# Kernel optimization log

Measured on AMD Instinct MI355X. Metric: run time of the kernel, lower is better.

## Reference

```python
import jax, jax.numpy as jnp
import numpy as np


def _rope_tables(N, d, base=10000.0):
    # LLaMA-style: freqs over even dims, interleaved (pairs) layout
    inv = 1.0 / (base ** (np.arange(0, d, 2)[: d // 2].astype(np.float32) / d))
    ang = np.outer(np.arange(N, dtype=np.float32), inv)  # [N, d/2]
    return jnp.asarray(np.cos(ang), jnp.float32), jnp.asarray(np.sin(ang), jnp.float32)


def _apply_rope(x, cos, sin):
    # x: [B, h, N, d]; pairs layout (..., d/2, 2)
    B, h, N, d = x.shape
    xs = x.reshape(B, h, N, d // 2, 2)
    x0, x1 = xs[..., 0], xs[..., 1]
    c = cos[None, None, :, :]
    s = sin[None, None, :, :]
    o0 = x0 * c - x1 * s
    o1 = x1 * c + x0 * s
    return jnp.stack([o0, o1], axis=-1).reshape(B, h, N, d)


def _neighborhood_attn(q, k, v, window, scale):
    # q,k,v: [B, h, H, W, d]; NATTEN-style clamped window of size window x window
    B, h, H, W, d = q.shape
    r = window // 2
    ih = jnp.clip(jnp.arange(H) - r, 0, H - window)[:, None] + jnp.arange(window)  # [H, w]
    iw = jnp.clip(jnp.arange(W) - r, 0, W - window)[:, None] + jnp.arange(window)  # [W, w]
    # gather windows: [B, h, H, W, w, w, d]
    kwin = k[:, :, ih[:, None, :, None], iw[None, :, None, :], :]
    vwin = v[:, :, ih[:, None, :, None], iw[None, :, None, :], :]
    attn = jnp.einsum('bhijd,bhijpqd->bhijpq', q, kwin) * scale
    attn = jax.nn.softmax(attn.reshape(B, h, H, W, window * window), axis=-1)
    out = jnp.einsum('bhijp,bhijpd->bhijd', attn,
                     vwin.reshape(B, h, H, W, window * window, d))
    return out  # [B, h, H, W, d]


def setup_inputs() -> dict:
    key = jax.random.key(0)
    k1, k2, k3 = jax.random.split(key, 3)
    B, H, W, C = 2, 56, 56, 256
    N = H * W
    x = jax.random.normal(k1, (B, N, C), dtype=jnp.float32)
    Wqkv = jax.random.normal(k2, (C, 3 * C), dtype=jnp.float32) * 0.02
    Wproj = jax.random.normal(k3, (C, C), dtype=jnp.float32) * 0.02
    bproj = jnp.zeros((C,), dtype=jnp.float32)
    return {"x": x, "Wqkv": Wqkv, "Wproj": Wproj, "bproj": bproj, "H": H, "W": W}


def reference(x, Wqkv, Wproj, bproj, H, W):
    head_dim = 32
    window = 7
    B, N, C = x.shape
    heads = C // head_dim
    scale = head_dim ** (-0.5)

    qkv = (x @ Wqkv).reshape(B, N, 3, heads, head_dim)
    qkv = jnp.transpose(qkv, (2, 0, 3, 1, 4))  # [3, B, h, N, d]
    q, k, v = qkv[0], qkv[1], qkv[2]

    cos, sin = _rope_tables(N, head_dim)
    q = _apply_rope(q, cos, sin)
    k = _apply_rope(k, cos, sin)

    q = q.reshape(B, heads, H, W, head_dim)
    k = k.reshape(B, heads, H, W, head_dim)
    v = v.reshape(B, heads, H, W, head_dim)

    out = _neighborhood_attn(q, k, v, window, scale)  # [B, h, H, W, d]
    out = out.reshape(B, heads, N, head_dim)
    out = jnp.transpose(out, (0, 2, 1, 3)).reshape(B, N, C)
    return out @ Wproj + bproj
```

## Files before the change

### kernel.cpp

```cpp
#include <hip/hip_runtime.h>
#include <hip/hip_bf16.h>

#define HH 56
#define WW 56
#define NPOS 3136
#define BATCH 2
#define HEADS 8

typedef __attribute__((ext_vector_type(4))) float floatx4;
typedef __attribute__((ext_vector_type(8))) short short8;

static __device__ __forceinline__ ushort f2b(float f) {
    __hip_bfloat16 h = __float2bfloat16(f);
    return *reinterpret_cast<ushort*>(&h);
}
static __device__ __forceinline__ float b2f(ushort u) {
    return __uint_as_float(((uint)u) << 16);
}

static __device__ __forceinline__ void async16(const ushort* g, ushort* l) {
    __builtin_amdgcn_global_load_lds(
        (const __attribute__((address_space(1))) unsigned int*)g,
        (__attribute__((address_space(3))) unsigned int*)l, 16, 0, 0);
}

__constant__ float INVF[16] = {
    1.0f,   0.5623413251903491f,   0.31622776601683794f,   0.17782794100389228f,
    0.1f,   0.05623413251903491f,  0.031622776601683794f,  0.017782794100389228f,
    0.01f,  0.005623413251903491f, 0.0031622776601683794f, 0.0017782794100389228f,
    0.001f, 0.0005623413251903491f,0.00031622776601683794f,0.00017782794100389228f
};


__global__ __launch_bounds__(256) void prepass(
    const float* __restrict__ x, const float* __restrict__ wqkv,
    const float* __restrict__ wproj,
    ushort* __restrict__ xb, ushort* __restrict__ wqkvT,
    ushort* __restrict__ wprojT, float* __restrict__ ropeT)
{
    __shared__ ushort Ls[64 * 65];
    const int bid = blockIdx.x, t = threadIdx.x;
    if (bid < 1568) {
        int i = (bid * 256 + t) * 4;
        float4 v = *(const float4*)&x[i];
        ushort4 h; h.x = f2b(v.x); h.y = f2b(v.y); h.z = f2b(v.z); h.w = f2b(v.w);
        *(ushort4*)&xb[i] = h;
    } else if (bid < 1764) {
        int i = (bid - 1568) * 256 + t;
        int pos = i >> 4, pr = i & 15;
        float s, c;
        __sincosf((float)pos * INVF[pr], &s, &c);
        ropeT[2 * i] = c; ropeT[2 * i + 1] = s;
    } else if (bid < 1812) {
        int l = bid - 1764;
        int nb = (l % 12) * 64, kb = (l / 12) * 64;
#pragma unroll
        for (int i = 0; i < 16; ++i) {
            int e = t + 256 * i, kk = e >> 6, nn = e & 63;
            Ls[kk * 65 + nn] = f2b(wqkv[(size_t)(kb + kk) * 768 + nb + nn]);
        }
        __syncthreads();
#pragma unroll
        for (int i = 0; i < 16; ++i) {
            int e = t + 256 * i, nn = e >> 6, kk = e & 63;
            wqkvT[(size_t)(nb + nn) * 256 + kb + kk] = Ls[kk * 65 + nn];
        }
    } else {
        int l = bid - 1812;
        int nb = (l & 3) * 64, kb = (l >> 2) * 64;
#pragma unroll
        for (int i = 0; i < 16; ++i) {
            int e = t + 256 * i, kk = e >> 6, nn = e & 63;
            Ls[kk * 65 + nn] = f2b(wproj[(size_t)(kb + kk) * 256 + nb + nn]);
        }
        __syncthreads();
#pragma unroll
        for (int i = 0; i < 16; ++i) {
            int e = t + 256 * i, nn = e >> 6, kk = e & 63;
            wprojT[(size_t)(nb + nn) * 256 + kb + kk] = Ls[kk * 65 + nn];
        }
    }
}

__global__ __launch_bounds__(256) void qkv_fast(
    const ushort* __restrict__ xb, const ushort* __restrict__ wqkvT,
    const float* __restrict__ ropeT,
    float* __restrict__ qa, ushort* __restrict__ kws, ushort* __restrict__ vws)
{
    __shared__ ushort Ab[128 * 32];
    __shared__ ushort Bb[128 * 32];
    const int t = threadIdx.x;
    const int lane = t & 63, wv = t >> 6;
    const int qm = lane & 15, quad = lane >> 4;
    const int m0 = blockIdx.y * 128, n0 = blockIdx.x * 128;
    const int wr = wv >> 1, wc = wv & 1;
    const int srow = lane >> 2, scol = (lane & 3) * 8;

    floatx4 acc[4][4];
#pragma unroll
    for (int i = 0; i < 4; ++i)
#pragma unroll
        for (int j = 0; j < 4; ++j) acc[i][j] = (floatx4){0.f, 0.f, 0.f, 0.f};

    for (int k0 = 0; k0 < 256; k0 += 32) {
#pragma unroll
        for (int j = 0; j < 2; ++j) {
            int rbase = wv * 32 + j * 16;
            async16(&xb[(size_t)(m0 + rbase + srow) * 256 + k0 + scol], &Ab[rbase * 32]);
            async16(&wqkvT[(size_t)(n0 + rbase + srow) * 256 + k0 + scol], &Bb[rbase * 32]);
        }
        __syncthreads();
        short8 af[4], bf[4];
#pragma unroll
        for (int mt = 0; mt < 4; ++mt)
            af[mt] = *(const short8*)&Ab[(wr * 64 + mt * 16 + qm) * 32 + quad * 8];
#pragma unroll
        for (int nt = 0; nt < 4; ++nt)
            bf[nt] = *(const short8*)&Bb[(wc * 64 + nt * 16 + qm) * 32 + quad * 8];
#pragma unroll
        for (int mt = 0; mt < 4; ++mt)
#pragma unroll
            for (int nt = 0; nt < 4; ++nt)
                acc[mt][nt] = __builtin_amdgcn_mfma_f32_16x16x32_bf16(af[mt], bf[nt], acc[mt][nt], 0, 0, 0);
        __syncthreads();
    }

    const int whichB = n0 >> 8;
#pragma unroll
    for (int mt = 0; mt < 4; ++mt) {
#pragma unroll
        for (int r = 0; r < 4; ++r) {
            int m = m0 + wr * 64 + mt * 16 + quad * 4 + r;
            int b = (m >= NPOS) ? 1 : 0;
            int pos = m - b * NPOS;
            float c0 = 0.f, s0 = 0.f, c1 = 0.f, s1 = 0.f;
            if (whichB < 2) {
                float2 t0 = *(const float2*)&ropeT[(pos * 16 + (qm >> 1)) * 2];
                float2 t1 = *(const float2*)&ropeT[(pos * 16 + 8 + (qm >> 1)) * 2];
                c0 = t0.x; s0 = t0.y; c1 = t1.x; s1 = t1.y;
            }
#pragma unroll
            for (int nt = 0; nt < 4; ++nt) {
                int c = n0 + wc * 64 + nt * 16 + qm;
                int head = (c >> 5) & 7;
                int d = (nt & 1) * 16 + qm;
                float val = acc[mt][nt][r];
                if (whichB < 2) {
                    float other = __shfl_xor(val, 1);
                    float cf = (nt & 1) ? c1 : c0, sf = (nt & 1) ? s1 : s0;
                    val = (lane & 1) ? (val * cf + other * sf)
                                     : (val * cf - other * sf);
                }
                if (whichB == 0) {
                    qa[(size_t)m * 256 + head * 32 + d] = val;
                } else {
                    ushort* dst = (whichB == 1) ? kws : vws;
                    dst[(size_t)(((b << 3) + head) * NPOS + pos) * 32 + d] = f2b(val);
                }
            }
        }
    }
}

__global__ __launch_bounds__(256) void proj_fast(
    const ushort* __restrict__ wprojT, const float* __restrict__ bias, float* out)
{
    __shared__ ushort Ap[64 * 264];
    __shared__ ushort Bb[64 * 32];
    const int t = threadIdx.x;
    const int lane = t & 63, wv = t >> 6;
    const int qm = lane & 15, quad = lane >> 4;
    const int n0 = blockIdx.x * 64, m0 = blockIdx.y * 64;
    const int wr = wv >> 1, wc = wv & 1;
    const int srow = lane >> 2, scol = (lane & 3) * 8;

    {
        int row = t >> 2, cb = (t & 3) * 64;
        const float4* src = (const float4*)&out[(size_t)(m0 + row) * 256 + cb];
#pragma unroll
        for (int i = 0; i < 16; ++i) {
            float4 v = src[i];
            ushort4 h; h.x = f2b(v.x); h.y = f2b(v.y); h.z = f2b(v.z); h.w = f2b(v.w);
            *(ushort4*)&Ap[row * 264 + cb + i * 4] = h;
        }
    }

    floatx4 acc[2][2];
#pragma unroll
    for (int i = 0; i < 2; ++i)
#pragma unroll
        for (int j = 0; j < 2; ++j) acc[i][j] = (floatx4){0.f, 0.f, 0.f, 0.f};

    for (int k0 = 0; k0 < 256; k0 += 32) {
        int rbase = wv * 16;
        async16(&wprojT[(size_t)(n0 + rbase + srow) * 256 + k0 + scol], &Bb[rbase * 32]);
        __syncthreads();
        short8 af[2], bf[2];
#pragma unroll
        for (int mt = 0; mt < 2; ++mt)
            af[mt] = *(const short8*)&Ap[(wr * 32 + mt * 16 + qm) * 264 + k0 + quad * 8];
#pragma unroll
        for (int nt = 0; nt < 2; ++nt)
            bf[nt] = *(const short8*)&Bb[(wc * 32 + nt * 16 + qm) * 32 + quad * 8];
#pragma unroll
        for (int mt = 0; mt < 2; ++mt)
#pragma unroll
            for (int nt = 0; nt < 2; ++nt)
                acc[mt][nt] = __builtin_amdgcn_mfma_f32_16x16x32_bf16(af[mt], bf[nt], acc[mt][nt], 0, 0, 0);
        __syncthreads();
    }

#pragma unroll
    for (int nt = 0; nt < 2; ++nt) {
        int c = n0 + wc * 32 + nt * 16 + qm;
        float bv = bias[c];
#pragma unroll
        for (int mt = 0; mt < 2; ++mt) {
#pragma unroll
            for (int r = 0; r < 4; ++r) {
                int m = m0 + wr * 32 + mt * 16 + quad * 4 + r;
                out[(size_t)m * 256 + c] = acc[mt][nt][r] + bv;
            }
        }
    }
}

__global__ __launch_bounds__(256) void nattn(
    const ushort* __restrict__ kws, const ushort* __restrict__ vws, float* qa)
{
    __shared__ ushort Ksm[196 * 32];
    __shared__ ushort Vsm[196 * 32];
    const int t = threadIdx.x;
    const int bh = blockIdx.y;
    const int b = bh >> 3, head = bh & 7;
    const int ti = blockIdx.x / 7, tj = blockIdx.x % 7;
    const int ty0 = ti * 8, tx0 = tj * 8;
    const int r0 = min(max(ty0 - 3, 0), HH - 14);
    const int c0 = min(max(tx0 - 3, 0), WW - 14);
    const ushort* kbase = kws + (size_t)bh * NPOS * 32;
    const ushort* vbase = vws + (size_t)bh * NPOS * 32;

    for (int idx = t; idx < 196 * 4; idx += 256) {
        int p = idx >> 2, ch = idx & 3;
        int g = ((r0 + p / 14) * WW + (c0 + p % 14)) * 32 + ch * 8;
        *(uint4*)&Ksm[p * 32 + ch * 8] = *(const uint4*)&kbase[g];
        *(uint4*)&Vsm[p * 32 + ch * 8] = *(const uint4*)&vbase[g];
    }
    __syncthreads();

    const int lane = t & 63, wv = t >> 6;
    const int qsub = lane & 15, part = lane >> 4;
    const int qi = wv * 16 + qsub;
    const int qy = ty0 + (qi >> 3), qx = tx0 + (qi & 7);
    const int pos = qy * WW + qx;
    float* qptr = qa + (size_t)(b * NPOS + pos) * 256 + head * 32;

    float qf[32];
#pragma unroll
    for (int c4 = 0; c4 < 8; ++c4) {
        float4 v = *(const float4*)&qptr[c4 * 4];
        qf[4 * c4] = v.x; qf[4 * c4 + 1] = v.y; qf[4 * c4 + 2] = v.z; qf[4 * c4 + 3] = v.w;
    }

    const int rs = min(max(qy - 3, 0), HH - 7) - r0;
    const int cs = min(max(qx - 3, 0), WW - 7) - c0;

    float sarr[13];
    float mx = -1e30f;
#pragma unroll
    for (int j = 0; j < 13; ++j) {
        int kk = part + 4 * j;
        sarr[j] = -1e30f;
        if (kk < 49) {
            int kp = (rs + kk / 7) * 14 + (cs + kk % 7);
            const uint4* Kp = (const uint4*)&Ksm[kp * 32];
            float s = 0.f;
#pragma unroll
            for (int c8 = 0; c8 < 4; ++c8) {
                uint4 u = Kp[c8];
                const float* qv = qf + 8 * c8;
                s += qv[0] * b2f((ushort)u.x) + qv[1] * b2f((ushort)(u.x >> 16));
                s += qv[2] * b2f((ushort)u.y) + qv[3] * b2f((ushort)(u.y >> 16));
                s += qv[4] * b2f((ushort)u.z) + qv[5] * b2f((ushort)(u.z >> 16));
                s += qv[6] * b2f((ushort)u.w) + qv[7] * b2f((ushort)(u.w >> 16));
            }
            s *= 0.17677669529663687f;
            sarr[j] = s;
            mx = fmaxf(mx, s);
        }
    }
    mx = fmaxf(mx, __shfl_xor(mx, 16));
    mx = fmaxf(mx, __shfl_xor(mx, 32));

    float sum = 0.f;
    float facc[32];
#pragma unroll
    for (int c = 0; c < 32; ++c) facc[c] = 0.f;
#pragma unroll
    for (int j = 0; j < 13; ++j) {
        int kk = part + 4 * j;
        if (kk < 49) {
            float e = __expf(sarr[j] - mx);
            sum += e;
            int kp = (rs + kk / 7) * 14 + (cs + kk % 7);
            const uint4* Vp = (const uint4*)&Vsm[kp * 32];
#pragma unroll
            for (int c8 = 0; c8 < 4; ++c8) {
                uint4 u = Vp[c8];
                float* fv = facc + 8 * c8;
                fv[0] += e * b2f((ushort)u.x); fv[1] += e * b2f((ushort)(u.x >> 16));
                fv[2] += e * b2f((ushort)u.y); fv[3] += e * b2f((ushort)(u.y >> 16));
                fv[4] += e * b2f((ushort)u.z); fv[5] += e * b2f((ushort)(u.z >> 16));
                fv[6] += e * b2f((ushort)u.w); fv[7] += e * b2f((ushort)(u.w >> 16));
            }
        }
    }
    sum += __shfl_xor(sum, 16);
    sum += __shfl_xor(sum, 32);
#pragma unroll
    for (int c = 0; c < 32; ++c) {
        facc[c] += __shfl_xor(facc[c], 16);
        facc[c] += __shfl_xor(facc[c], 32);
    }

    if (part == 0) {
        float inv = 1.f / sum;
#pragma unroll
        for (int c4 = 0; c4 < 8; ++c4) {
            float4 o;
            o.x = facc[4 * c4]     * inv;
            o.y = facc[4 * c4 + 1] * inv;
            o.z = facc[4 * c4 + 2] * inv;
            o.w = facc[4 * c4 + 3] * inv;
            *(float4*)&qptr[c4 * 4] = o;
        }
    }
}

__global__ __launch_bounds__(256) void qkv_fb(
    const float* __restrict__ x, const float* __restrict__ w,
    float* __restrict__ qa, ushort* __restrict__ kws, ushort* __restrict__ vws)
{
    __shared__ ushort Asm[64 * 40];
    __shared__ ushort Bsm[64 * 40];
    const int t = threadIdx.x;
    const int m0 = blockIdx.y * 64;
    const int n0 = blockIdx.x * 64;
    const int lane = t & 63, wv = t >> 6;
    const int qm = lane & 15, quad = lane >> 4;

    floatx4 acc[4];
#pragma unroll
    for (int i = 0; i < 4; ++i) acc[i] = (floatx4){0.f, 0.f, 0.f, 0.f};

    for (int k0 = 0; k0 < 256; k0 += 32) {
#pragma unroll
        for (int i = 0; i < 2; ++i) {
            int p = t + 256 * i;
            int row = p >> 3, f4 = p & 7;
            float4 v = *(const float4*)&x[(size_t)(m0 + row) * 256 + k0 + f4 * 4];
            ushort4 h;
            h.x = f2b(v.x); h.y = f2b(v.y); h.z = f2b(v.z); h.w = f2b(v.w);
            *(ushort4*)&Asm[row * 40 + f4 * 4] = h;
        }
#pragma unroll
        for (int i = 0; i < 8; ++i) {
            int e = t + 256 * i;
            int kk = e >> 6, nn = e & 63;
            Bsm[nn * 40 + kk] = f2b(w[(size_t)(k0 + kk) * 768 + n0 + nn]);
        }
        __syncthreads();
        short8 af = *(const short8*)&Asm[(wv * 16 + qm) * 40 + quad * 8];
#pragma unroll
        for (int nt = 0; nt < 4; ++nt) {
            short8 bf = *(const short8*)&Bsm[(nt * 16 + qm) * 40 + quad * 8];
            acc[nt] = __builtin_amdgcn_mfma_f32_16x16x32_bf16(af, bf, acc[nt], 0, 0, 0);
        }
        __syncthreads();
    }

    const int whichB = n0 >> 8;
#pragma unroll
    for (int r = 0; r < 4; ++r) {
        int m = m0 + wv * 16 + quad * 4 + r;
        int b = (m >= NPOS) ? 1 : 0;
        int pos = m - b * NPOS;
        float cf[2], sf[2];
        if (whichB < 2) {
            float posf = (float)pos;
            __sincosf(posf * INVF[qm >> 1], &sf[0], &cf[0]);
            __sincosf(posf * INVF[8 + (qm >> 1)], &sf[1], &cf[1]);
        }
#pragma unroll
        for (int nt = 0; nt < 4; ++nt) {
            int par = nt & 1;
            int d = par * 16 + qm;
            int head = ((n0 >> 5) & 7) + (nt >> 1);
            float val = acc[nt][r];
            if (whichB < 2) {
                float other = __shfl_xor(val, 1);
                val = (lane & 1) ? (val * cf[par] + other * sf[par])
                                 : (val * cf[par] - other * sf[par]);
            }
            if (whichB == 0) {
                qa[(size_t)m * 256 + head * 32 + d] = val;
            } else {
                ushort* dst = (whichB == 1) ? kws : vws;
                dst[(size_t)(((b << 3) + head) * NPOS + pos) * 32 + d] = f2b(val);
            }
        }
    }
}

__global__ __launch_bounds__(256) void proj_fb(
    const float* __restrict__ w, const float* __restrict__ bias, float* out)
{
    __shared__ ushort Apad[64 * 264];
    __shared__ ushort Bsm[256 * 40];
    const int t = threadIdx.x;
    const int m0 = blockIdx.x * 64;
    const int lane = t & 63, wv = t >> 6;
    const int qm = lane & 15, quad = lane >> 4;

    {
        int row = t >> 2, cb = (t & 3) * 64;
        const float4* src = (const float4*)&out[(size_t)(m0 + row) * 256 + cb];
#pragma unroll
        for (int i = 0; i < 16; ++i) {
            float4 v = src[i];
            ushort4 h;
            h.x = f2b(v.x); h.y = f2b(v.y); h.z = f2b(v.z); h.w = f2b(v.w);
            *(ushort4*)&Apad[row * 264 + cb + i * 4] = h;
        }
    }

    floatx4 acc[4][4];
#pragma unroll
    for (int i = 0; i < 4; ++i)
#pragma unroll
        for (int j = 0; j < 4; ++j) acc[i][j] = (floatx4){0.f, 0.f, 0.f, 0.f};

    __syncthreads();

    for (int k0 = 0; k0 < 256; k0 += 32) {
#pragma unroll
        for (int i = 0; i < 32; ++i) {
            int e = t + 256 * i;
            int kk = e >> 8, nn = e & 255;
            Bsm[nn * 40 + kk] = f2b(w[(size_t)(k0 + kk) * 256 + nn]);
        }
        __syncthreads();
        short8 af[4];
#pragma unroll
        for (int mt = 0; mt < 4; ++mt)
            af[mt] = *(const short8*)&Apad[(mt * 16 + qm) * 264 + k0 + quad * 8];
#pragma unroll
        for (int nt = 0; nt < 4; ++nt) {
            short8 bf = *(const short8*)&Bsm[(wv * 64 + nt * 16 + qm) * 40 + quad * 8];
#pragma unroll
            for (int mt = 0; mt < 4; ++mt)
                acc[mt][nt] = __builtin_amdgcn_mfma_f32_16x16x32_bf16(af[mt], bf, acc[mt][nt], 0, 0, 0);
        }
        __syncthreads();
    }

#pragma unroll
    for (int nt = 0; nt < 4; ++nt) {
        int c = wv * 64 + nt * 16 + qm;
        float bv = bias[c];
#pragma unroll
        for (int mt = 0; mt < 4; ++mt) {
#pragma unroll
            for (int r = 0; r < 4; ++r) {
                int m = m0 + mt * 16 + quad * 4 + r;
                out[(size_t)m * 256 + c] = acc[mt][nt][r] + bv;
            }
        }
    }
}

extern "C" void kernel_launch(void* const* d_in, const int* in_sizes, int n_in,
                              void* d_out, int out_size, void* d_ws, size_t ws_size,
                              hipStream_t stream)
{
    const float* x     = (const float*)d_in[0];
    const float* wqkv  = (const float*)d_in[1];
    const float* wproj = (const float*)d_in[2];
    const float* bproj = (const float*)d_in[3];
    float* out = (float*)d_out;
    char* ws = (char*)d_ws;

    if (ws_size >= 10559488ull) {
        ushort* xb     = (ushort*)(ws);
        ushort* wqkvT  = (ushort*)(ws + 3211264);
        ushort* wprojT = (ushort*)(ws + 3604480);
        float*  ropeT  = (float*) (ws + 3735552);
        ushort* kws    = (ushort*)(ws + 4136960);
        ushort* vws    = (ushort*)(ws + 7348224);

        hipLaunchKernelGGL(prepass, dim3(1828), dim3(256), 0, stream,
                           x, wqkv, wproj, xb, wqkvT, wprojT, ropeT);
        hipLaunchKernelGGL(qkv_fast, dim3(6, 49), dim3(256), 0, stream,
                           xb, wqkvT, ropeT, out, kws, vws);
        hipLaunchKernelGGL(nattn, dim3(49, BATCH * HEADS), dim3(256), 0, stream,
                           kws, vws, out);
        hipLaunchKernelGGL(proj_fast, dim3(4, 98), dim3(256), 0, stream,
                           wprojT, bproj, out);
    } else {
        ushort* kws = (ushort*)ws;
        ushort* vws = (ushort*)(ws + 3211264);
        hipLaunchKernelGGL(qkv_fb, dim3(12, 98), dim3(256), 0, stream,
                           x, wqkv, out, kws, vws);
        hipLaunchKernelGGL(nattn, dim3(49, BATCH * HEADS), dim3(256), 0, stream,
                           kws, vws, out);
        hipLaunchKernelGGL(proj_fb, dim3(98), dim3(256), 0, stream,
                           wproj, bproj, out);
    }
}
```

Baseline: 138.5 us.

## Fuse x bf16 conversion into QKV GEMM and pass bf16 intermediates between kernels

Drops the prepass step that converts x to bf16 and instead converts fp32 x to bf16 inside the QKV GEMM's A-tile load. Q and the attention output are now stored as bf16 in workspace rather than fp32 in the output buffer. The projection kernel can then load A tiles with async global-to-LDS copies. Together this cuts intermediate memory traffic, but the A loads become synchronous register loads, and the new path needs a larger workspace, so the old nattn is kept as a fallback.

Measured after the change: 130.3 us. 5.9% less time.

```diff
diff --git a/kernel.cpp b/kernel.cpp
--- a/kernel.cpp
+++ b/kernel.cpp
@@ -32,27 +32,21 @@
 };
 
 
-__global__ __launch_bounds__(256) void prepass(
-    const float* __restrict__ x, const float* __restrict__ wqkv,
-    const float* __restrict__ wproj,
-    ushort* __restrict__ xb, ushort* __restrict__ wqkvT,
-    ushort* __restrict__ wprojT, float* __restrict__ ropeT)
+__global__ __launch_bounds__(256) void prep(
+    const float* __restrict__ wqkv, const float* __restrict__ wproj,
+    ushort* __restrict__ wqkvT, ushort* __restrict__ wprojT,
+    float* __restrict__ ropeT)
 {
     __shared__ ushort Ls[64 * 65];
     const int bid = blockIdx.x, t = threadIdx.x;
-    if (bid < 1568) {
-        int i = (bid * 256 + t) * 4;
-        float4 v = *(const float4*)&x[i];
-        ushort4 h; h.x = f2b(v.x); h.y = f2b(v.y); h.z = f2b(v.z); h.w = f2b(v.w);
-        *(ushort4*)&xb[i] = h;
-    } else if (bid < 1764) {
-        int i = (bid - 1568) * 256 + t;
+    if (bid < 196) {
+        int i = bid * 256 + t;
         int pos = i >> 4, pr = i & 15;
         float s, c;
         __sincosf((float)pos * INVF[pr], &s, &c);
         ropeT[2 * i] = c; ropeT[2 * i + 1] = s;
-    } else if (bid < 1812) {
-        int l = bid - 1764;
+    } else if (bid < 244) {
+        int l = bid - 196;
         int nb = (l % 12) * 64, kb = (l / 12) * 64;
 #pragma unroll
         for (int i = 0; i < 16; ++i) {
@@ -66,7 +60,7 @@
             wqkvT[(size_t)(nb + nn) * 256 + kb + kk] = Ls[kk * 65 + nn];
         }
     } else {
-        int l = bid - 1812;
+        int l = bid - 244;
         int nb = (l & 3) * 64, kb = (l >> 2) * 64;
 #pragma unroll
         for (int i = 0; i < 16; ++i) {
@@ -83,9 +77,9 @@
 }
 
 __global__ __launch_bounds__(256) void qkv_fast(
-    const ushort* __restrict__ xb, const ushort* __restrict__ wqkvT,
+    const float* __restrict__ x, const ushort* __restrict__ wqkvT,
     const float* __restrict__ ropeT,
-    float* __restrict__ qa, ushort* __restrict__ kws, ushort* __restrict__ vws)
+    ushort* __restrict__ qb, ushort* __restrict__ kws, ushort* __restrict__ vws)
 {
     __shared__ ushort Ab[128 * 32];
     __shared__ ushort Bb[128 * 32];
@@ -95,6 +89,7 @@
     const int m0 = blockIdx.y * 128, n0 = blockIdx.x * 128;
     const int wr = wv >> 1, wc = wv & 1;
     const int srow = lane >> 2, scol = (lane & 3) * 8;
+    const int arow = t >> 1, aseg = (t & 1) * 16;
 
     floatx4 acc[4][4];
 #pragma unroll
@@ -103,10 +98,16 @@
         for (int j = 0; j < 4; ++j) acc[i][j] = (floatx4){0.f, 0.f, 0.f, 0.f};
 
     for (int k0 = 0; k0 < 256; k0 += 32) {
+#pragma unroll
+        for (int i = 0; i < 4; ++i) {
+            int col = aseg + i * 4;
+            float4 v = *(const float4*)&x[(size_t)(m0 + arow) * 256 + k0 + col];
+            ushort4 h; h.x = f2b(v.x); h.y = f2b(v.y); h.z = f2b(v.z); h.w = f2b(v.w);
+            *(ushort4*)&Ab[arow * 32 + col] = h;
+        }
 #pragma unroll
         for (int j = 0; j < 2; ++j) {
             int rbase = wv * 32 + j * 16;
-            async16(&xb[(size_t)(m0 + rbase + srow) * 256 + k0 + scol], &Ab[rbase * 32]);
             async16(&wqkvT[(size_t)(n0 + rbase + srow) * 256 + k0 + scol], &Bb[rbase * 32]);
         }
         __syncthreads();
@@ -152,7 +153,7 @@
                                      : (val * cf - other * sf);
                 }
                 if (whichB == 0) {
-                    qa[(size_t)m * 256 + head * 32 + d] = val;
+                    qb[(size_t)m * 256 + head * 32 + d] = f2b(val);
                 } else {
                     ushort* dst = (whichB == 1) ? kws : vws;
                     dst[(size_t)(((b << 3) + head) * NPOS + pos) * 32 + d] = f2b(val);
@@ -162,71 +163,9 @@
     }
 }
 
-__global__ __launch_bounds__(256) void proj_fast(
-    const ushort* __restrict__ wprojT, const float* __restrict__ bias, float* out)
-{
-    __shared__ ushort Ap[64 * 264];
-    __shared__ ushort Bb[64 * 32];
-    const int t = threadIdx.x;
-    const int lane = t & 63, wv = t >> 6;
-    const int qm = lane & 15, quad = lane >> 4;
-    const int n0 = blockIdx.x * 64, m0 = blockIdx.y * 64;
-    const int wr = wv >> 1, wc = wv & 1;
-    const int srow = lane >> 2, scol = (lane & 3) * 8;
-
-    {
-        int row = t >> 2, cb = (t & 3) * 64;
-        const float4* src = (const float4*)&out[(size_t)(m0 + row) * 256 + cb];
-#pragma unroll
-        for (int i = 0; i < 16; ++i) {
-            float4 v = src[i];
-            ushort4 h; h.x = f2b(v.x); h.y = f2b(v.y); h.z = f2b(v.z); h.w = f2b(v.w);
-            *(ushort4*)&Ap[row * 264 + cb + i * 4] = h;
-        }
-    }
-
-    floatx4 acc[2][2];
-#pragma unroll
-    for (int i = 0; i < 2; ++i)
-#pragma unroll
-        for (int j = 0; j < 2; ++j) acc[i][j] = (floatx4){0.f, 0.f, 0.f, 0.f};
-
-    for (int k0 = 0; k0 < 256; k0 += 32) {
-        int rbase = wv * 16;
-        async16(&wprojT[(size_t)(n0 + rbase + srow) * 256 + k0 + scol], &Bb[rbase * 32]);
-        __syncthreads();
-        short8 af[2], bf[2];
-#pragma unroll
-        for (int mt = 0; mt < 2; ++mt)
-            af[mt] = *(const short8*)&Ap[(wr * 32 + mt * 16 + qm) * 264 + k0 + quad * 8];
-#pragma unroll
-        for (int nt = 0; nt < 2; ++nt)
-            bf[nt] = *(const short8*)&Bb[(wc * 32 + nt * 16 + qm) * 32 + quad * 8];
-#pragma unroll
-        for (int mt = 0; mt < 2; ++mt)
-#pragma unroll
-            for (int nt = 0; nt < 2; ++nt)
-                acc[mt][nt] = __builtin_amdgcn_mfma_f32_16x16x32_bf16(af[mt], bf[nt], acc[mt][nt], 0, 0, 0);
-        __syncthreads();
-    }
-
-#pragma unroll
-    for (int nt = 0; nt < 2; ++nt) {
-        int c = n0 + wc * 32 + nt * 16 + qm;
-        float bv = bias[c];
-#pragma unroll
-        for (int mt = 0; mt < 2; ++mt) {
-#pragma unroll
-            for (int r = 0; r < 4; ++r) {
-                int m = m0 + wr * 32 + mt * 16 + quad * 4 + r;
-                out[(size_t)m * 256 + c] = acc[mt][nt][r] + bv;
-            }
-        }
-    }
-}
-
 __global__ __launch_bounds__(256) void nattn(
-    const ushort* __restrict__ kws, const ushort* __restrict__ vws, float* qa)
+    const ushort* __restrict__ kws, const ushort* __restrict__ vws,
+    const ushort* __restrict__ qb, ushort* __restrict__ ab)
 {
     __shared__ ushort Ksm[196 * 32];
     __shared__ ushort Vsm[196 * 32];
@@ -253,13 +192,16 @@
     const int qi = wv * 16 + qsub;
     const int qy = ty0 + (qi >> 3), qx = tx0 + (qi & 7);
     const int pos = qy * WW + qx;
-    float* qptr = qa + (size_t)(b * NPOS + pos) * 256 + head * 32;
+    const size_t qoff = (size_t)(b * NPOS + pos) * 256 + head * 32;
 
     float qf[32];
-#pragma unroll
-    for (int c4 = 0; c4 < 8; ++c4) {
-        float4 v = *(const float4*)&qptr[c4 * 4];
-        qf[4 * c4] = v.x; qf[4 * c4 + 1] = v.y; qf[4 * c4 + 2] = v.z; qf[4 * c4 + 3] = v.w;
+    {
+        const uint* q4 = (const uint*)(qb + qoff);
+#pragma unroll
+        for (int c2 = 0; c2 < 16; ++c2) {
+            uint u = q4[c2];
+            qf[2 * c2] = b2f((ushort)u); qf[2 * c2 + 1] = b2f((ushort)(u >> 16));
+        }
     }
 
     const int rs = min(max(qy - 3, 0), HH - 7) - r0;
@@ -325,14 +267,66 @@
 
     if (part == 0) {
         float inv = 1.f / sum;
-#pragma unroll
-        for (int c4 = 0; c4 < 8; ++c4) {
-            float4 o;
-            o.x = facc[4 * c4]     * inv;
-            o.y = facc[4 * c4 + 1] * inv;
-            o.z = facc[4 * c4 + 2] * inv;
-            o.w = facc[4 * c4 + 3] * inv;
-            *(float4*)&qptr[c4 * 4] = o;
+        uint* op = (uint*)(ab + qoff);
+#pragma unroll
+        for (int c2 = 0; c2 < 16; ++c2) {
+            uint lo = f2b(facc[2 * c2] * inv);
+            uint hi = f2b(facc[2 * c2 + 1] * inv);
+            op[c2] = lo | (hi << 16);
+        }
+    }
+}
+
+__global__ __launch_bounds__(256) void proj_fast(
+    const ushort* __restrict__ ab, const ushort* __restrict__ wprojT,
+    const float* __restrict__ bias, float* __restrict__ out)
+{
+    __shared__ ushort Ap[64 * 32];
+    __shared__ ushort Bp[64 * 32];
+    const int t = threadIdx.x;
+    const int lane = t & 63, wv = t >> 6;
+    const int qm = lane & 15, quad = lane >> 4;
+    const int n0 = blockIdx.x * 64, m0 = blockIdx.y * 64;
+    const int wr = wv >> 1, wc = wv & 1;
+    const int srow = lane >> 2, scol = (lane & 3) * 8;
+
+    floatx4 acc[2][2];
+#pragma unroll
+    for (int i = 0; i < 2; ++i)
+#pragma unroll
+        for (int j = 0; j < 2; ++j) acc[i][j] = (floatx4){0.f, 0.f, 0.f, 0.f};
+
+    for (int k0 = 0; k0 < 256; k0 += 32) {
+        int rbase = wv * 16;
+        async16(&ab[(size_t)(m0 + rbase + srow) * 256 + k0 + scol], &Ap[rbase * 32]);
+        async16(&wprojT[(size_t)(n0 + rbase + srow) * 256 + k0 + scol], &Bp[rbase * 32]);
+        __syncthreads();
+        short8 af[2], bf[2];
+#pragma unroll
+        for (int mt = 0; mt < 2; ++mt)
+            af[mt] = *(const short8*)&Ap[(wr * 32 + mt * 16 + qm) * 32 + quad * 8];
+#pragma unroll
+        for (int nt = 0; nt < 2; ++nt)
+            bf[nt] = *(const short8*)&Bp[(wc * 32 + nt * 16 + qm) * 32 + quad * 8];
+#pragma unroll
+        for (int mt = 0; mt < 2; ++mt)
+#pragma unroll
+            for (int nt = 0; nt < 2; ++nt)
+                acc[mt][nt] = __builtin_amdgcn_mfma_f32_16x16x32_bf16(af[mt], bf[nt], acc[mt][nt], 0, 0, 0);
+        __syncthreads();
+    }
+
+#pragma unroll
+    for (int nt = 0; nt < 2; ++nt) {
+        int c = n0 + wc * 32 + nt * 16 + qm;
+        float bv = bias[c];
+#pragma unroll
+        for (int mt = 0; mt < 2; ++mt) {
+#pragma unroll
+            for (int r = 0; r < 4; ++r) {
+                int m = m0 + wr * 32 + mt * 16 + quad * 4 + r;
+                out[(size_t)m * 256 + c] = acc[mt][nt][r] + bv;
+            }
         }
     }
 }
@@ -412,6 +406,116 @@
     }
 }
 
+__global__ __launch_bounds__(256) void nattn_fb(
+    const ushort* __restrict__ kws, const ushort* __restrict__ vws, float* qa)
+{
+    __shared__ ushort Ksm[196 * 32];
+    __shared__ ushort Vsm[196 * 32];
+    const int t = threadIdx.x;
+    const int bh = blockIdx.y;
+    const int b = bh >> 3, head = bh & 7;
+    const int ti = blockIdx.x / 7, tj = blockIdx.x % 7;
+    const int ty0 = ti * 8, tx0 = tj * 8;
+    const int r0 = min(max(ty0 - 3, 0), HH - 14);
+    const int c0 = min(max(tx0 - 3, 0), WW - 14);
+    const ushort* kbase = kws + (size_t)bh * NPOS * 32;
+    const ushort* vbase = vws + (size_t)bh * NPOS * 32;
+
+    for (int idx = t; idx < 196 * 4; idx += 256) {
+        int p = idx >> 2, ch = idx & 3;
+        int g = ((r0 + p / 14) * WW + (c0 + p % 14)) * 32 + ch * 8;
+        *(uint4*)&Ksm[p * 32 + ch * 8] = *(const uint4*)&kbase[g];
+        *(uint4*)&Vsm[p * 32 + ch * 8] = *(const uint4*)&vbase[g];
+    }
+    __syncthreads();
+
+    const int lane = t & 63, wv = t >> 6;
+    const int qsub = lane & 15, part = lane >> 4;
+    const int qi = wv * 16 + qsub;
+    const int qy = ty0 + (qi >> 3), qx = tx0 + (qi & 7);
+    const int pos = qy * WW + qx;
+    float* qptr = qa + (size_t)(b * NPOS + pos) * 256 + head * 32;
+
+    float qf[32];
+#pragma unroll
+    for (int c4 = 0; c4 < 8; ++c4) {
+        float4 v = *(const float4*)&qptr[c4 * 4];
+        qf[4 * c4] = v.x; qf[4 * c4 + 1] = v.y; qf[4 * c4 + 2] = v.z; qf[4 * c4 + 3] = v.w;
+    }
+
+    const int rs = min(max(qy - 3, 0), HH - 7) - r0;
+    const int cs = min(max(qx - 3, 0), WW - 7) - c0;
+
+    float sarr[13];
+    float mx = -1e30f;
+#pragma unroll
+    for (int j = 0; j < 13; ++j) {
+        int kk = part + 4 * j;
+        sarr[j] = -1e30f;
+        if (kk < 49) {
+            int kp = (rs + kk / 7) * 14 + (cs + kk % 7);
+            const uint4* Kp = (const uint4*)&Ksm[kp * 32];
+            float s = 0.f;
+#pragma unroll
+            for (int c8 = 0; c8 < 4; ++c8) {
+                uint4 u = Kp[c8];
+                const float* qv = qf + 8 * c8;
+                s += qv[0] * b2f((ushort)u.x) + qv[1] * b2f((ushort)(u.x >> 16));
+                s += qv[2] * b2f((ushort)u.y) + qv[3] * b2f((ushort)(u.y >> 16));
+                s += qv[4] * b2f((ushort)u.z) + qv[5] * b2f((ushort)(u.z >> 16));
+                s += qv[6] * b2f((ushort)u.w) + qv[7] * b2f((ushort)(u.w >> 16));
+            }
+            s *= 0.17677669529663687f;
+            sarr[j] = s;
+            mx = fmaxf(mx, s);
+        }
+    }
+    mx = fmaxf(mx, __shfl_xor(mx, 16));
+    mx = fmaxf(mx, __shfl_xor(mx, 32));
+
+    float sum = 0.f;
+    float facc[32];
+#pragma unroll
+    for (int c = 0; c < 32; ++c) facc[c] = 0.f;
+#pragma unroll
+    for (int j = 0; j < 13; ++j) {
+        int kk = part + 4 * j;
+        if (kk < 49) {
+            float e = __expf(sarr[j] - mx);
+            sum += e;
+            int kp = (rs + kk / 7) * 14 + (cs + kk % 7);
+            const uint4* Vp = (const uint4*)&Vsm[kp * 32];
+#pragma unroll
+            for (int c8 = 0; c8 < 4; ++c8) {
+                uint4 u = Vp[c8];
+                float* fv = facc + 8 * c8;
+                fv[0] += e * b2f((ushort)u.x); fv[1] += e * b2f((ushort)(u.x >> 16));
+                fv[2] += e * b2f((ushort)u.y); fv[3] += e * b2f((ushort)(u.y >> 16));
+                fv[4] += e * b2f((ushort)u.z); fv[5] += e * b2f((ushort)(u.z >> 16));
+                fv[6] += e * b2f((ushort)u.w); fv[7] += e * b2f((ushort)(u.w >> 16));
+            }
+        }
+    }
+    sum += __shfl_xor(sum, 16);
+    sum += __shfl_xor(sum, 32);
+#pragma unroll
+    for (int c = 0; c < 32; ++c) {
+        facc[c] += __shfl_xor(facc[c], 16);
+        facc[c] += __shfl_xor(facc[c], 32);
+    }
+
+    if (part == 0) {
+        float inv = 1.f / sum;
+#pragma unroll
+        for (int c4 = 0; c4 < 8; ++c4) {
+            float4 o;
+            o.x = facc[4 * c4] * inv; o.y = facc[4 * c4 + 1] * inv;
+            o.z = facc[4 * c4 + 2] * inv; o.w = facc[4 * c4 + 3] * inv;
+            *(float4*)&qptr[c4 * 4] = o;
+        }
+    }
+}
+
 __global__ __launch_bounds__(256) void proj_fb(
     const float* __restrict__ w, const float* __restrict__ bias, float* out)
 {
@@ -490,28 +594,29 @@
     float* out = (float*)d_out;
     char* ws = (char*)d_ws;
 
-    if (ws_size >= 10559488ull) {
-        ushort* xb     = (ushort*)(ws);
-        ushort* wqkvT  = (ushort*)(ws + 3211264);
-        ushort* wprojT = (ushort*)(ws + 3604480);
-        float*  ropeT  = (float*) (ws + 3735552);
+    if (ws_size >= 13770752ull) {
+        ushort* wqkvT  = (ushort*)(ws);
+        ushort* wprojT = (ushort*)(ws + 393216);
+        float*  ropeT  = (float*) (ws + 524288);
+        ushort* qb     = (ushort*)(ws + 925696);
         ushort* kws    = (ushort*)(ws + 4136960);
         ushort* vws    = (ushort*)(ws + 7348224);
-
-        hipLaunchKernelGGL(prepass, dim3(1828), dim3(256), 0, stream,
-                           x, wqkv, wproj, xb, wqkvT, wprojT, ropeT);
+        ushort* ab     = (ushort*)(ws + 10559488);
+
+        hipLaunchKernelGGL(prep, dim3(260), dim3(256), 0, stream,
+                           wqkv, wproj, wqkvT, wprojT, ropeT);
         hipLaunchKernelGGL(qkv_fast, dim3(6, 49), dim3(256), 0, stream,
-                           xb, wqkvT, ropeT, out, kws, vws);
+                           x, wqkvT, ropeT, qb, kws, vws);
         hipLaunchKernelGGL(nattn, dim3(49, BATCH * HEADS), dim3(256), 0, stream,
-                           kws, vws, out);
+                           kws, vws, qb, ab);
         hipLaunchKernelGGL(proj_fast, dim3(4, 98), dim3(256), 0, stream,
-                           wprojT, bproj, out);
+                           ab, wprojT, bproj, out);
     } else {
         ushort* kws = (ushort*)ws;
         ushort* vws = (ushort*)(ws + 3211264);
         hipLaunchKernelGGL(qkv_fb, dim3(12, 98), dim3(256), 0, stream,
                            x, wqkv, out, kws, vws);
-        hipLaunchKernelGGL(nattn, dim3(49, BATCH * HEADS), dim3(256), 0, stream,
+        hipLaunchKernelGGL(nattn_fb, dim3(49, BATCH * HEADS), dim3(256), 0, stream,
                            kws, vws, out);
         hipLaunchKernelGGL(proj_fb, dim3(98), dim3(256), 0, stream,
                            wproj, bproj, out);
```
